# Performance work log

Measured on AMD Instinct MI355X. Metric: run time of the kernel, lower is better.

The kernel has to match this reference:

```python
import jax, jax.numpy as jnp
import numpy as np

TEM = 6  # forward hardcodes Tem=6 for index building; init default Tem=6 for weights


def _build_index(H, W, Tem):
    # Faithful port of _build_matrix_index: row edges per phase, col edges per phase,
    # then cross-phase edges linking corresponding pixels of adjacent phases.
    raw = jnp.arange(W, dtype=jnp.int32)[None, :] + jnp.arange(H, dtype=jnp.int32)[:, None] * W  # [H,W]
    pw = W // Tem
    phases = [raw[:, i * pw:(i + 1) * pw] for i in range(Tem)]
    rows = [jnp.stack([p[:-1, :], p[1:, :]], axis=2).reshape(-1, 2) for p in phases]
    cols = [jnp.stack([p[:, :-1], p[:, 1:]], axis=2).reshape(-1, 2) for p in phases]
    cross = [jnp.stack([phases[i], phases[i + 1]], axis=2).reshape(-1, 2) for i in range(Tem - 1)]
    return jnp.concatenate(rows + cols + cross, axis=0)  # [E,2]


def _build_weight_norm2(fm, Tem):
    # Faithful port of _build_feature_weight_norm2_distance, INCLUDING the original
    # per-phase [row,col] interleaved ordering (which differs from the index ordering).
    B, D, H, W = fm.shape
    pw = W // Tem
    phases = [fm[:, :, :, i * pw:(i + 1) * pw] for i in range(Tem)]
    ws = []
    for p in phases:
        wr = ((p[:, :, :-1, :] - p[:, :, 1:, :]) ** 2).sum(axis=1).reshape(B, -1)
        wc = ((p[:, :, :, :-1] - p[:, :, :, 1:]) ** 2).sum(axis=1).reshape(B, -1)
        ws.extend([wr, wc])
    for i in range(Tem - 1):
        ws.append(((phases[i] - phases[i + 1]) ** 2).sum(axis=1).reshape(B, -1))
    return jnp.concatenate(ws, axis=1)  # [B,E]


def _mst_single(u, v, w, V):
    # Vectorized Boruvka MST with pointer-jumping union-find (jit-compatible,
    # fixed round count >= ceil(log2 V)). Ties broken by a globally unique edge rank.
    E = u.shape[0]
    order = jnp.argsort(w)  # stable -> unique rank per edge
    rank = jnp.zeros(E, jnp.int32).at[order].set(jnp.arange(E, dtype=jnp.int32))
    n_rounds = int(np.ceil(np.log2(max(V, 2)))) + 1
    idx_v = jnp.arange(V, dtype=jnp.int32)

    def round_fn(carry, _):
        comp, mask = carry
        cu, cv = comp[u], comp[v]
        active = cu != cv
        key = jnp.where(active, rank, E)  # E = sentinel 'no edge'
        mk = jnp.minimum(jax.ops.segment_min(key, cu, num_segments=V),
                         jax.ops.segment_min(key, cv, num_segments=V))  # min rank per component
        has = mk < E
        sel = order[jnp.clip(mk, 0, E - 1)]  # chosen edge index per component
        a, b = cu[sel], cv[sel]
        other = jnp.where(a == idx_v, b, a)
        parent = jnp.where(has, other, idx_v)
        # break mutual 2-cycles: smaller-index component becomes root
        gp = parent[parent]
        parent = jnp.where((gp == idx_v) & (idx_v < parent), idx_v, parent)
        # full path compression via pointer jumping
        parent = jax.lax.while_loop(lambda p: jnp.any(p[p] != p), lambda p: p[p], parent)
        comp = parent[comp]
        mask = mask.at[jnp.where(has, sel, E)].set(True)  # slot E is scratch
        return (comp, mask), None

    comp0 = jnp.arange(V, dtype=jnp.int32)
    mask0 = jnp.zeros(E + 1, dtype=bool)
    (comp, mask), _ = jax.lax.scan(round_fn, (comp0, mask0), None, length=n_rounds)
    mask = mask[:E]
    # grid graph is connected -> exactly V-1 selected edges; emit sorted edge ids
    tree = jnp.sort(jnp.where(mask, jnp.arange(E, dtype=jnp.int32), E))[: V - 1]
    return tree  # [V-1] int32


def setup_inputs() -> dict:
    key = jax.random.key(0)
    guide_in = jax.random.normal(key, (4, 64, 288, 432), dtype=jnp.float32)
    return {"guide_in": guide_in}


def reference(guide_in):
    B, C, H, W = guide_in.shape
    V = H * W
    index = _build_index(H, W, TEM)  # [E,2], same for every batch element
    weight = _build_weight_norm2(guide_in, TEM)  # [B,E]
    u, v = index[:, 0], index[:, 1]
    tree = jax.vmap(lambda ww: _mst_single(u, v, ww, V))(weight)  # [B, V-1]
    return tree
```

## Files before the change

kernel.cpp:

```cpp
#include <hip/hip_runtime.h>
#include <cstdint>
#include <cstddef>

#define NB 4
#define NC 64
#define HH 288
#define WW 432
#define PW 72
#define NV (HH*WW)
#define R_PER ((HH-1)*PW)
#define C_PER (HH*(PW-1))
#define X_PER (HH*PW)
#define PAIRW (R_PER + C_PER)
#define ROWS_TOT (6*R_PER)
#define ROWCOL (6*PAIRW)
#define NE (ROWCOL + 5*X_PER)
#define NEB ((NE + 255)/256)
#define NEP (NEB*256)
#define NWORDS_P (NEP/32)
#define NTREE (NV-1)
#define NROUNDS 18
#define CHUNK 4096
#define NCHUNK ((NE + CHUNK - 1)/CHUNK)

typedef unsigned long long ull;

__device__ __forceinline__ void index_uv(int e, int& u, int& v) {
    if (e < ROWS_TOT) {
        int t = e / R_PER, l = e - t * R_PER;
        int h = l / PW, x = l - h * PW;
        u = h * WW + t * PW + x; v = u + WW;
    } else if (e < ROWCOL) {
        int q = e - ROWS_TOT;
        int t = q / C_PER, l = q - t * C_PER;
        int h = l / (PW-1), x = l - h * (PW-1);
        u = h * WW + t * PW + x; v = u + 1;
    } else {
        int q = e - ROWCOL;
        int t = q / X_PER, l = q - t * X_PER;
        int h = l / PW, x = l - h * PW;
        u = h * WW + t * PW + x; v = u + PW;
    }
}

__device__ __forceinline__ int rootOf(const int* __restrict__ par, int c) {
    while (true) {
        int p = par[c];
        if (p == c) return c;
        int pp = par[p];
        if (pp == c) return c < p ? c : p;
        c = p;
    }
}

__global__ __launch_bounds__(256) void init_kernel(int* comp, int* parent,
                                                   ull* minkey, unsigned char* mask,
                                                   unsigned* aliveW,
                                                   int* found, int* done) {
    int i = blockIdx.x * 256 + threadIdx.x;
    int b = blockIdx.y;
    if (i < NV) {
        comp[(size_t)b*NV + i] = i;
        parent[(size_t)b*NV + i] = i;
        minkey[(size_t)b*NV + i] = ~0ULL;
    }
    if (i < NE) mask[(size_t)b*NE + i] = 0;
    if (i < NWORDS_P) aliveW[(size_t)b*NWORDS_P + i] = 0xffffffffu;
    if (b == 0 && i < NB) { found[i] = 1; found[NB + i] = 0; done[i] = 0; }
}

__global__ __launch_bounds__(256) void key0_kernel(const float* __restrict__ fm,
                                                   ull* __restrict__ keys,
                                                   ull* __restrict__ minkey) {
    int i = blockIdx.x * 256 + threadIdx.x;
    int b = blockIdx.y;
    if (i >= NV) return;
    int h = i / WW, x = i - h * WW;
    int t = x / PW, xr = x - t * PW;
    bool hv = (h < HH-1);
    bool hh = (xr < PW-1);
    bool hx = (x < WW-PW);
    int ov = hv ? WW : 0;
    int oh = hh ? 1  : 0;
    int ox = hx ? PW : 0;
    const float* base = fm + (size_t)b * NC * NV + i;
    float sv = 0.f, sh_ = 0.f, sx = 0.f;
    #pragma unroll 8
    for (int ch = 0; ch < NC; ++ch) {
        const float* p = base + (size_t)ch * NV;
        float f0 = p[0];
        float dv = f0 - p[ov];
        float dh = f0 - p[oh];
        float dx = f0 - p[ox];
        sv += dv * dv; sh_ += dh * dh; sx += dx * dx;
    }
    ull* mk = minkey + (size_t)b * NV;
    ull* ky = keys + (size_t)b * NE;
    if (hv) {
        int e = t * PAIRW + h * PW + xr;
        ull k = ((ull)__float_as_uint(sv) << 32) | (unsigned int)e;
        ky[e] = k;
        int u, v; index_uv(e, u, v);
        atomicMin(&mk[u], k); atomicMin(&mk[v], k);
    }
    if (hh) {
        int e = t * PAIRW + R_PER + h * (PW-1) + xr;
        ull k = ((ull)__float_as_uint(sh_) << 32) | (unsigned int)e;
        ky[e] = k;
        int u, v; index_uv(e, u, v);
        atomicMin(&mk[u], k); atomicMin(&mk[v], k);
    }
    if (hx) {
        int e = ROWCOL + t * X_PER + h * PW + xr;
        ull k = ((ull)__float_as_uint(sx) << 32) | (unsigned int)e;
        ky[e] = k;
        int u, v; index_uv(e, u, v);
        atomicMin(&mk[u], k); atomicMin(&mk[v], k);
    }
}

__global__ __launch_bounds__(256) void scan_kernel(const ull* __restrict__ keys,
                                                   int* __restrict__ comp,
                                                   const int* __restrict__ parent,
                                                   ull* __restrict__ minkey,
                                                   unsigned* __restrict__ aliveW,
                                                   int* __restrict__ foundCur,
                                                   const int* __restrict__ done) {
    int e = blockIdx.x * 256 + threadIdx.x;
    int b = blockIdx.y;
    if (done[b]) return;
    const int lane = threadIdx.x & 63;
    unsigned* aw = aliveW + (size_t)b * NWORDS_P;
    bool was = false, live = false;
    int cu = 0, cv = 0;
    if (e < NE) was = (aw[e >> 5] >> (e & 31)) & 1;
    if (was) {
        const int* par = parent + (size_t)b * NV;
        int* cmp = comp + (size_t)b * NV;
        int u, v; index_uv(e, u, v);
        cu = rootOf(par, cmp[u]); if (cmp[u] != cu) cmp[u] = cu;
        cv = rootOf(par, cmp[v]); if (cmp[v] != cv) cmp[v] = cv;
        live = (cu != cv);
    }
    if (live) {
        ull k = keys[(size_t)b * NE + e];
        ull* mk = minkey + (size_t)b * NV;
        if (k < mk[cu]) atomicMin(&mk[cu], k);
        if (k < mk[cv]) atomicMin(&mk[cv], k);
    }
    ull ball = __ballot(live ? 1 : 0);
    ull ballWas = __ballot(was ? 1 : 0);
    if (ball != ballWas) {
        int wbase = (blockIdx.x * 256 + (threadIdx.x & ~63)) >> 5;
        if (lane == 0)  aw[wbase]     = (unsigned)ball;
        if (lane == 32) aw[wbase + 1] = (unsigned)(ball >> 32);
    }
    if (ball && lane == __ffsll((long long)ball) - 1)
        foundCur[b] = 1;
}

__global__ __launch_bounds__(256) void select_kernel(const int* __restrict__ comp,
                                                     int* __restrict__ parent,
                                                     ull* __restrict__ minkey,
                                                     unsigned char* __restrict__ mask,
                                                     const int* __restrict__ foundCur,
                                                     int* __restrict__ foundNext,
                                                     int* __restrict__ done) {
    int c = blockIdx.x * 256 + threadIdx.x;
    int b = blockIdx.y;
    int fc = foundCur[b];
    if (c == 0) {
        foundNext[b] = 0;
        if (fc == 0) done[b] = 1;
    }
    if (fc == 0) return;
    if (c >= NV) return;
    size_t off = (size_t)b * NV;
    ull k = minkey[off + c];
    int par = c;
    if (k != ~0ULL) {
        minkey[off + c] = ~0ULL;
        int e = (int)(k & 0xffffffffu);
        mask[(size_t)b * NE + e] = 1;
        int u, v; index_uv(e, u, v);
        int cu = comp[off + u], cv = comp[off + v];
        par = (cu == c) ? cv : cu;
    }
    if (parent[off + c] != par) parent[off + c] = par;
}

__global__ __launch_bounds__(256) void count_kernel(const unsigned char* __restrict__ mask,
                                                    int* __restrict__ counts) {
    int b = blockIdx.y, ck = blockIdx.x, t = threadIdx.x;
    const unsigned char* m = mask + (size_t)b * NE;
    int base_e = ck * CHUNK + t * 16;
    int cnt = 0;
    #pragma unroll
    for (int i = 0; i < 16; ++i) {
        int e = base_e + i;
        if (e < NE && m[e]) cnt++;
    }
    __shared__ int sh[256];
    sh[t] = cnt;
    __syncthreads();
    for (int o = 128; o > 0; o >>= 1) {
        if (t < o) sh[t] += sh[t + o];
        __syncthreads();
    }
    if (t == 0) counts[b * NCHUNK + ck] = sh[0];
}

__global__ __launch_bounds__(256) void write_kernel(const unsigned char* __restrict__ mask,
                                                    const int* __restrict__ counts,
                                                    int* __restrict__ out) {
    int b = blockIdx.y, ck = blockIdx.x, t = threadIdx.x;
    __shared__ int sh[256];
    __shared__ int shOff[128];
    shOff[t & 127] = 0;
    __syncthreads();
    if (t < NCHUNK && t < ck) shOff[t] = counts[b * NCHUNK + t];
    __syncthreads();
    for (int o = 64; o > 0; o >>= 1) {
        if (t < o) shOff[t] += shOff[t + o];
        __syncthreads();
    }
    int blockOff = shOff[0];

    const unsigned char* m = mask + (size_t)b * NE;
    int base_e = ck * CHUNK + t * 16;
    int cnt = 0;
    #pragma unroll
    for (int i = 0; i < 16; ++i) {
        int e = base_e + i;
        if (e < NE && m[e]) cnt++;
    }
    sh[t] = cnt;
    __syncthreads();
    for (int o = 1; o < 256; o <<= 1) {
        int v = 0;
        if (t >= o) v = sh[t - o];
        __syncthreads();
        sh[t] += v;
        __syncthreads();
    }
    int pos = blockOff + (sh[t] - cnt);
    for (int i = 0; i < 16; ++i) {
        int e = base_e + i;
        if (e < NE && m[e]) {
            if (pos < NTREE) out[(size_t)b * NTREE + pos] = e;
            pos++;
        }
    }
}

extern "C" void kernel_launch(void* const* d_in, const int* in_sizes, int n_in,
                              void* d_out, int out_size, void* d_ws, size_t ws_size,
                              hipStream_t stream) {
    const float* fm = (const float*)d_in[0];
    int* out = (int*)d_out;

    char* ws = (char*)d_ws;
    size_t off = 0;
    auto alloc = [&](size_t bytes) -> void* {
        void* p = ws + off;
        off += (bytes + 255) & ~(size_t)255;
        return p;
    };
    ull* keys    = (ull*)alloc((size_t)NB * NE * 8);
    ull* minkey  = (ull*)alloc((size_t)NB * NV * 8);
    int* comp    = (int*)alloc((size_t)NB * NV * 4);
    int* parent  = (int*)alloc((size_t)NB * NV * 4);
    unsigned char* mask = (unsigned char*)alloc((size_t)NB * NE);
    unsigned* aliveW = (unsigned*)alloc((size_t)NB * NWORDS_P * 4);
    int* counts  = (int*)alloc((size_t)NB * NCHUNK * 4);
    int* found   = (int*)alloc(2 * NB * 4);
    int* done    = (int*)alloc(NB * 4);

    dim3 blk(256);
    dim3 gE(NEB, NB);
    dim3 gV((NV + 255) / 256, NB);

    init_kernel<<<gE, blk, 0, stream>>>(comp, parent, minkey, mask, aliveW, found, done);
    key0_kernel<<<gV, blk, 0, stream>>>(fm, keys, minkey);

    select_kernel<<<gV, blk, 0, stream>>>(comp, parent, minkey, mask,
                                          found, found + NB, done);
    for (int r = 1; r < NROUNDS; ++r) {
        int* fCur  = found + (r & 1) * NB;
        int* fNext = found + ((r + 1) & 1) * NB;
        scan_kernel<<<gE, blk, 0, stream>>>(keys, comp, parent, minkey, aliveW,
                                            fCur, done);
        select_kernel<<<gV, blk, 0, stream>>>(comp, parent, minkey, mask,
                                              fCur, fNext, done);
    }

    count_kernel<<<dim3(NCHUNK, NB), blk, 0, stream>>>(mask, counts);
    write_kernel<<<dim3(NCHUNK, NB), blk, 0, stream>>>(mask, counts, out);
}
```

Baseline: 628.0 us.

## Replace alive-edge bitmask with compacted edge worklists in Boruvka rounds

The per-round scan no longer sweeps every edge against an alive bitmask. After the first full scan, the live (cross-component) edges are compacted into a worklist with block-level ballot prefix sums and a global atomic counter. Later rounds iterate only over that list with a fixed grid of 128 blocks per batch and write a new compacted list through double buffering. This cuts per-round work as components merge, at the cost of extra list memory, atomic counter traffic, a fixed small grid that may underuse the GPU in early rounds, and indirect, less coalesced edge accesses.

After: 636.9 us. Within noise of the previous version (+1.4%).

```diff
diff --git a/kernel.cpp b/kernel.cpp
--- a/kernel.cpp
+++ b/kernel.cpp
@@ -16,12 +16,12 @@
 #define ROWCOL (6*PAIRW)
 #define NE (ROWCOL + 5*X_PER)
 #define NEB ((NE + 255)/256)
-#define NEP (NEB*256)
-#define NWORDS_P (NEP/32)
 #define NTREE (NV-1)
 #define NROUNDS 18
 #define CHUNK 4096
 #define NCHUNK ((NE + CHUNK - 1)/CHUNK)
+#define CSTR 32
+#define SLB 128
 
 typedef unsigned long long ull;
 
@@ -55,8 +55,7 @@
 
 __global__ __launch_bounds__(256) void init_kernel(int* comp, int* parent,
                                                    ull* minkey, unsigned char* mask,
-                                                   unsigned* aliveW,
-                                                   int* found, int* done) {
+                                                   int* cnt, int* found, int* done) {
     int i = blockIdx.x * 256 + threadIdx.x;
     int b = blockIdx.y;
     if (i < NV) {
@@ -65,7 +64,7 @@
         minkey[(size_t)b*NV + i] = ~0ULL;
     }
     if (i < NE) mask[(size_t)b*NE + i] = 0;
-    if (i < NWORDS_P) aliveW[(size_t)b*NWORDS_P + i] = 0xffffffffu;
+    if (b == 0 && i < 2*NB*CSTR) cnt[i] = 0;
     if (b == 0 && i < NB) { found[i] = 1; found[NB + i] = 0; done[i] = 0; }
 }
 
@@ -119,44 +118,119 @@
     }
 }
 
-__global__ __launch_bounds__(256) void scan_kernel(const ull* __restrict__ keys,
-                                                   int* __restrict__ comp,
-                                                   const int* __restrict__ parent,
-                                                   ull* __restrict__ minkey,
-                                                   unsigned* __restrict__ aliveW,
-                                                   int* __restrict__ foundCur,
-                                                   const int* __restrict__ done) {
-    int e = blockIdx.x * 256 + threadIdx.x;
-    int b = blockIdx.y;
+__global__ __launch_bounds__(256) void scan_full_kernel(const ull* __restrict__ keys,
+                                                        int* __restrict__ comp,
+                                                        const int* __restrict__ parent,
+                                                        ull* __restrict__ minkey,
+                                                        int* __restrict__ list0,
+                                                        int* __restrict__ cnt,
+                                                        int* __restrict__ fCur) {
+    const int tid = threadIdx.x;
+    const int b = blockIdx.y;
+    const int e = blockIdx.x * 256 + tid;
+    const bool valid = e < NE;
+    const size_t offV = (size_t)b * NV;
+    const int* par = parent + offV;
+    int* cmp = comp + offV;
+    ull* mk = minkey + offV;
+    const ull* ky = keys + (size_t)b * NE;
+
+    bool live = false;
+    if (valid) {
+        int u, v; index_uv(e, u, v);
+        int cu0 = cmp[u], cv0 = cmp[v];
+        ull k = ky[e];
+        int cu = rootOf(par, cu0); if (cu0 != cu) cmp[u] = cu;
+        int cv = rootOf(par, cv0); if (cv0 != cv) cmp[v] = cv;
+        live = (cu != cv);
+        if (live) {
+            if (k < mk[cu]) atomicMin(&mk[cu], k);
+            if (k < mk[cv]) atomicMin(&mk[cv], k);
+        }
+    }
+    __shared__ int s_wb[4];
+    __shared__ int s_bcnt;
+    __shared__ int s_gb;
+    ull ball = __ballot(live ? 1 : 0);
+    if (tid == 0) s_bcnt = 0;
+    __syncthreads();
+    if ((tid & 63) == 0) s_wb[tid >> 6] = ball ? atomicAdd(&s_bcnt, __popcll(ball)) : 0;
+    __syncthreads();
+    if (tid == 0 && s_bcnt) {
+        s_gb = atomicAdd(&cnt[b * CSTR], s_bcnt);
+        fCur[b] = 1;
+    }
+    __syncthreads();
+    if (live) {
+        int lane = tid & 63;
+        int pos = s_gb + s_wb[tid >> 6] + __popcll(ball & ((1ull << lane) - 1));
+        list0[(size_t)b * NE + pos] = e;
+    }
+}
+
+__global__ __launch_bounds__(256) void scan_list_kernel(const ull* __restrict__ keys,
+                                                        int* __restrict__ comp,
+                                                        const int* __restrict__ parent,
+                                                        ull* __restrict__ minkey,
+                                                        int* __restrict__ list0,
+                                                        int* __restrict__ list1,
+                                                        int* __restrict__ cnt,
+                                                        int rpar,
+                                                        int* __restrict__ fCur,
+                                                        const int* __restrict__ done) {
+    const int b = blockIdx.y;
     if (done[b]) return;
-    const int lane = threadIdx.x & 63;
-    unsigned* aw = aliveW + (size_t)b * NWORDS_P;
-    bool was = false, live = false;
-    int cu = 0, cv = 0;
-    if (e < NE) was = (aw[e >> 5] >> (e & 31)) & 1;
-    if (was) {
-        const int* par = parent + (size_t)b * NV;
-        int* cmp = comp + (size_t)b * NV;
-        int u, v; index_uv(e, u, v);
-        cu = rootOf(par, cmp[u]); if (cmp[u] != cu) cmp[u] = cu;
-        cv = rootOf(par, cmp[v]); if (cmp[v] != cv) cmp[v] = cv;
-        live = (cu != cv);
-    }
-    if (live) {
-        ull k = keys[(size_t)b * NE + e];
-        ull* mk = minkey + (size_t)b * NV;
-        if (k < mk[cu]) atomicMin(&mk[cu], k);
-        if (k < mk[cv]) atomicMin(&mk[cv], k);
-    }
-    ull ball = __ballot(live ? 1 : 0);
-    ull ballWas = __ballot(was ? 1 : 0);
-    if (ball != ballWas) {
-        int wbase = (blockIdx.x * 256 + (threadIdx.x & ~63)) >> 5;
-        if (lane == 0)  aw[wbase]     = (unsigned)ball;
-        if (lane == 32) aw[wbase + 1] = (unsigned)(ball >> 32);
-    }
-    if (ball && lane == __ffsll((long long)ball) - 1)
-        foundCur[b] = 1;
+    const int tid = threadIdx.x;
+    const int n = cnt[rpar * NB * CSTR + b * CSTR];
+    int* cw = &cnt[(rpar ^ 1) * NB * CSTR + b * CSTR];
+    const int* lr = (rpar ? list1 : list0) + (size_t)b * NE;
+    int* lw = (rpar ? list0 : list1) + (size_t)b * NE;
+    const size_t offV = (size_t)b * NV;
+    const int* par = parent + offV;
+    int* cmp = comp + offV;
+    ull* mk = minkey + offV;
+    const ull* ky = keys + (size_t)b * NE;
+
+    const int stride = SLB * 256;
+    const int nIter = (n + stride - 1) / stride;
+    __shared__ int s_wb[4];
+    __shared__ int s_bcnt;
+    __shared__ int s_gb;
+
+    for (int it = 0; it < nIter; ++it) {
+        int i = it * stride + blockIdx.x * 256 + tid;
+        bool valid = i < n;
+        bool live = false;
+        int e = 0;
+        if (valid) {
+            e = lr[i];
+            int u, v; index_uv(e, u, v);
+            int cu0 = cmp[u], cv0 = cmp[v];
+            ull k = ky[e];
+            int cu = rootOf(par, cu0); if (cu0 != cu) cmp[u] = cu;
+            int cv = rootOf(par, cv0); if (cv0 != cv) cmp[v] = cv;
+            live = (cu != cv);
+            if (live) {
+                if (k < mk[cu]) atomicMin(&mk[cu], k);
+                if (k < mk[cv]) atomicMin(&mk[cv], k);
+            }
+        }
+        ull ball = __ballot(live ? 1 : 0);
+        if (tid == 0) s_bcnt = 0;
+        __syncthreads();
+        if ((tid & 63) == 0) s_wb[tid >> 6] = ball ? atomicAdd(&s_bcnt, __popcll(ball)) : 0;
+        __syncthreads();
+        if (tid == 0 && s_bcnt) {
+            s_gb = atomicAdd(cw, s_bcnt);
+            fCur[b] = 1;
+        }
+        __syncthreads();
+        if (live) {
+            int lane = tid & 63;
+            int pos = s_gb + s_wb[tid >> 6] + __popcll(ball & ((1ull << lane) - 1));
+            lw[pos] = e;
+        }
+    }
 }
 
 __global__ __launch_bounds__(256) void select_kernel(const int* __restrict__ comp,
@@ -165,12 +239,15 @@
                                                      unsigned char* __restrict__ mask,
                                                      const int* __restrict__ foundCur,
                                                      int* __restrict__ foundNext,
-                                                     int* __restrict__ done) {
+                                                     int* __restrict__ done,
+                                                     int* __restrict__ cnt,
+                                                     int zpar) {
     int c = blockIdx.x * 256 + threadIdx.x;
     int b = blockIdx.y;
     int fc = foundCur[b];
     if (c == 0) {
         foundNext[b] = 0;
+        cnt[zpar * NB * CSTR + b * CSTR] = 0;
         if (fc == 0) done[b] = 1;
     }
     if (fc == 0) return;
@@ -271,7 +348,9 @@
     int* comp    = (int*)alloc((size_t)NB * NV * 4);
     int* parent  = (int*)alloc((size_t)NB * NV * 4);
     unsigned char* mask = (unsigned char*)alloc((size_t)NB * NE);
-    unsigned* aliveW = (unsigned*)alloc((size_t)NB * NWORDS_P * 4);
+    int* list0   = (int*)alloc((size_t)NB * NE * 4);
+    int* list1   = (int*)alloc((size_t)NB * NE * 4);
+    int* cnt     = (int*)alloc(2 * NB * CSTR * 4);
     int* counts  = (int*)alloc((size_t)NB * NCHUNK * 4);
     int* found   = (int*)alloc(2 * NB * 4);
     int* done    = (int*)alloc(NB * 4);
@@ -279,19 +358,25 @@
     dim3 blk(256);
     dim3 gE(NEB, NB);
     dim3 gV((NV + 255) / 256, NB);
-
-    init_kernel<<<gE, blk, 0, stream>>>(comp, parent, minkey, mask, aliveW, found, done);
+    dim3 gL(SLB, NB);
+
+    init_kernel<<<gE, blk, 0, stream>>>(comp, parent, minkey, mask, cnt, found, done);
     key0_kernel<<<gV, blk, 0, stream>>>(fm, keys, minkey);
 
     select_kernel<<<gV, blk, 0, stream>>>(comp, parent, minkey, mask,
-                                          found, found + NB, done);
-    for (int r = 1; r < NROUNDS; ++r) {
+                                          found, found + NB, done, cnt, 0);
+    scan_full_kernel<<<gE, blk, 0, stream>>>(keys, comp, parent, minkey,
+                                             list0, cnt, found + NB);
+    select_kernel<<<gV, blk, 0, stream>>>(comp, parent, minkey, mask,
+                                          found + NB, found, done, cnt, 1);
+    for (int r = 2; r < NROUNDS; ++r) {
         int* fCur  = found + (r & 1) * NB;
         int* fNext = found + ((r + 1) & 1) * NB;
-        scan_kernel<<<gE, blk, 0, stream>>>(keys, comp, parent, minkey, aliveW,
-                                            fCur, done);
+        scan_list_kernel<<<gL, blk, 0, stream>>>(keys, comp, parent, minkey,
+                                                 list0, list1, cnt, r & 1,
+                                                 fCur, done);
         select_kernel<<<gV, blk, 0, stream>>>(comp, parent, minkey, mask,
-                                              fCur, fNext, done);
+                                              fCur, fNext, done, cnt, r & 1);
     }
 
     count_kernel<<<dim3(NCHUNK, NB), blk, 0, stream>>>(mask, counts);
```
